# Performance work log

Measured on AMD Instinct MI355X. Metric: run time of the kernel, lower is better.

The kernel has to match this reference:

```python
import jax, jax.numpy as jnp
import numpy as np

B, K, N = 131072, 512, 1024  # batch, message bits, code bits


def setup_inputs() -> dict:
    key = jax.random.key(0)
    k1, k2 = jax.random.split(key)
    input_data = jax.random.randint(k1, (B, K), 0, 2).astype(jnp.float32)
    generator_matrix = jax.random.randint(k2, (N, K), 0, 2).astype(jnp.float32)
    return {"input_data": input_data, "generator_matrix": generator_matrix}


def reference(input_data, generator_matrix):
    # GF(2) encoding: (x @ G^T) mod 2
    # input_data: [B, K], generator_matrix: [N, K] -> out [B, N]
    prod = jnp.matmul(input_data, generator_matrix.T)
    return jnp.mod(prod, 2.0)
```

## Files before the change

### kernel.cpp

```cpp
#include <hip/hip_runtime.h>
#include <cstdint>


typedef float f32x4 __attribute__((ext_vector_type(4)));

__global__ void pack256_kernel(const float* __restrict__ in,
                               unsigned long long* __restrict__ out,
                               int nChunks) {
    const int chunk = blockIdx.x * (blockDim.x >> 6) + (threadIdx.x >> 6);
    const int lane = threadIdx.x & 63;
    if (chunk >= nChunks) return;
    const float4 v =
        reinterpret_cast<const float4*>(in + (size_t)chunk * 256)[lane];
    unsigned long long m0 = __ballot(v.x != 0.0f);
    unsigned long long m1 = __ballot(v.y != 0.0f);
    unsigned long long m2 = __ballot(v.z != 0.0f);
    unsigned long long m3 = __ballot(v.w != 0.0f);
    if (lane == 0) {
        unsigned long long* o = out + (size_t)chunk * 4;
        o[0] = m0; o[1] = m1; o[2] = m2; o[3] = m3;
    }
}

__global__ __launch_bounds__(256, 4) void gf2_fused_kernel(
    const float* __restrict__ x,
    const uint32_t* __restrict__ gp,
    float* __restrict__ out) {
    const int tid = threadIdx.x;
    const int lane = tid & 63;
    const long long b0 = (long long)blockIdx.x * 64;

    uint32_t g[4][16];
#pragma unroll
    for (int j = 0; j < 4; ++j) {
        const uint4* gr =
            reinterpret_cast<const uint4*>(gp + (size_t)(tid * 4 + j) * 16);
        uint4 a = gr[0], b = gr[1], c = gr[2], d = gr[3];
        g[j][0] = a.x;  g[j][1] = a.y;  g[j][2] = a.z;  g[j][3] = a.w;
        g[j][4] = b.x;  g[j][5] = b.y;  g[j][6] = b.z;  g[j][7] = b.w;
        g[j][8] = c.x;  g[j][9] = c.y;  g[j][10] = c.z; g[j][11] = c.w;
        g[j][12] = d.x; g[j][13] = d.y; g[j][14] = d.z; g[j][15] = d.w;
    }

    const float* xr = x + b0 * 512 + lane * 4;
    float4 p0 = *reinterpret_cast<const float4*>(xr);
    float4 p1 = *reinterpret_cast<const float4*>(xr + 256);

    for (int r = 0; r < 64; ++r) {
        const float4 c0 = p0, c1 = p1;
        if (r < 63) {
            xr += 512;
            p0 = *reinterpret_cast<const float4*>(xr);
            p1 = *reinterpret_cast<const float4*>(xr + 256);
        }
        unsigned long long m0 = __ballot(c0.x != 0.0f);
        unsigned long long m1 = __ballot(c0.y != 0.0f);
        unsigned long long m2 = __ballot(c0.z != 0.0f);
        unsigned long long m3 = __ballot(c0.w != 0.0f);
        unsigned long long m4 = __ballot(c1.x != 0.0f);
        unsigned long long m5 = __ballot(c1.y != 0.0f);
        unsigned long long m6 = __ballot(c1.z != 0.0f);
        unsigned long long m7 = __ballot(c1.w != 0.0f);
        const uint32_t xv[16] = {
            (uint32_t)m0, (uint32_t)(m0 >> 32),
            (uint32_t)m1, (uint32_t)(m1 >> 32),
            (uint32_t)m2, (uint32_t)(m2 >> 32),
            (uint32_t)m3, (uint32_t)(m3 >> 32),
            (uint32_t)m4, (uint32_t)(m4 >> 32),
            (uint32_t)m5, (uint32_t)(m5 >> 32),
            (uint32_t)m6, (uint32_t)(m6 >> 32),
            (uint32_t)m7, (uint32_t)(m7 >> 32)};

        uint32_t a0 = 0, a1 = 0, a2 = 0, a3 = 0;
#pragma unroll
        for (int i = 0; i < 16; ++i) {
            a0 ^= xv[i] & g[0][i];
            a1 ^= xv[i] & g[1][i];
            a2 ^= xv[i] & g[2][i];
            a3 ^= xv[i] & g[3][i];
        }
        f32x4 o;
        o.x = (float)(__popc(a0) & 1);
        o.y = (float)(__popc(a1) & 1);
        o.z = (float)(__popc(a2) & 1);
        o.w = (float)(__popc(a3) & 1);
        __builtin_nontemporal_store(
            o, reinterpret_cast<f32x4*>(out + (size_t)(b0 + r) * 1024) + tid);
    }
}

extern "C" void kernel_launch(void* const* d_in, const int* in_sizes, int n_in,
                              void* d_out, int out_size, void* d_ws, size_t ws_size,
                              hipStream_t stream) {
    const float* x = (const float*)d_in[0];
    const float* G = (const float*)d_in[1];
    float* out = (float*)d_out;

    const int B = 131072;
    unsigned long long* gp64 = (unsigned long long*)d_ws;

    pack256_kernel<<<512, 256, 0, stream>>>(G, gp64, 2048);
    gf2_fused_kernel<<<B / 64, 256, 0, stream>>>(
        x, (const uint32_t*)gp64, out);
}
```

Before: 187.4 us.

## Share bit-packed input rows across waves via LDS instead of redundant loads

Previously every wave in a block loaded and ballot-packed all 64 input rows, so each row was read from global memory four times. Now each wave packs a disjoint 16-row slice into shared memory, the block synchronizes, and all waves read the packed words from LDS for the XOR/AND loop. This cuts global and L2 read traffic for x by four, at the cost of a block barrier and losing overlap of loads with compute inside a wave.

```diff
diff --git a/kernel.cpp b/kernel.cpp
--- a/kernel.cpp
+++ b/kernel.cpp
@@ -26,8 +26,11 @@
     const float* __restrict__ x,
     const uint32_t* __restrict__ gp,
     float* __restrict__ out) {
+    __shared__ uint32_t xl[64 * 16];
+
     const int tid = threadIdx.x;
     const int lane = tid & 63;
+    const int wv = tid >> 6;
     const long long b0 = (long long)blockIdx.x * 64;
 
     uint32_t g[4][16];
@@ -42,35 +45,47 @@
         g[j][12] = d.x; g[j][13] = d.y; g[j][14] = d.z; g[j][15] = d.w;
     }
 
-    const float* xr = x + b0 * 512 + lane * 4;
-    float4 p0 = *reinterpret_cast<const float4*>(xr);
-    float4 p1 = *reinterpret_cast<const float4*>(xr + 256);
+    {
+        const float* xr = x + (b0 + wv * 16) * 512 + lane * 4;
+        float4 p0 = *reinterpret_cast<const float4*>(xr);
+        float4 p1 = *reinterpret_cast<const float4*>(xr + 256);
+        for (int r = 0; r < 16; ++r) {
+            const float4 c0 = p0, c1 = p1;
+            if (r < 15) {
+                xr += 512;
+                p0 = *reinterpret_cast<const float4*>(xr);
+                p1 = *reinterpret_cast<const float4*>(xr + 256);
+            }
+            unsigned long long m0 = __ballot(c0.x != 0.0f);
+            unsigned long long m1 = __ballot(c0.y != 0.0f);
+            unsigned long long m2 = __ballot(c0.z != 0.0f);
+            unsigned long long m3 = __ballot(c0.w != 0.0f);
+            unsigned long long m4 = __ballot(c1.x != 0.0f);
+            unsigned long long m5 = __ballot(c1.y != 0.0f);
+            unsigned long long m6 = __ballot(c1.z != 0.0f);
+            unsigned long long m7 = __ballot(c1.w != 0.0f);
+            if (lane == 0) {
+                uint4* dst = reinterpret_cast<uint4*>(&xl[(wv * 16 + r) * 16]);
+                dst[0] = make_uint4((uint32_t)m0, (uint32_t)(m0 >> 32),
+                                    (uint32_t)m1, (uint32_t)(m1 >> 32));
+                dst[1] = make_uint4((uint32_t)m2, (uint32_t)(m2 >> 32),
+                                    (uint32_t)m3, (uint32_t)(m3 >> 32));
+                dst[2] = make_uint4((uint32_t)m4, (uint32_t)(m4 >> 32),
+                                    (uint32_t)m5, (uint32_t)(m5 >> 32));
+                dst[3] = make_uint4((uint32_t)m6, (uint32_t)(m6 >> 32),
+                                    (uint32_t)m7, (uint32_t)(m7 >> 32));
+            }
+        }
+    }
+    __syncthreads();
 
     for (int r = 0; r < 64; ++r) {
-        const float4 c0 = p0, c1 = p1;
-        if (r < 63) {
-            xr += 512;
-            p0 = *reinterpret_cast<const float4*>(xr);
-            p1 = *reinterpret_cast<const float4*>(xr + 256);
-        }
-        unsigned long long m0 = __ballot(c0.x != 0.0f);
-        unsigned long long m1 = __ballot(c0.y != 0.0f);
-        unsigned long long m2 = __ballot(c0.z != 0.0f);
-        unsigned long long m3 = __ballot(c0.w != 0.0f);
-        unsigned long long m4 = __ballot(c1.x != 0.0f);
-        unsigned long long m5 = __ballot(c1.y != 0.0f);
-        unsigned long long m6 = __ballot(c1.z != 0.0f);
-        unsigned long long m7 = __ballot(c1.w != 0.0f);
-        const uint32_t xv[16] = {
-            (uint32_t)m0, (uint32_t)(m0 >> 32),
-            (uint32_t)m1, (uint32_t)(m1 >> 32),
-            (uint32_t)m2, (uint32_t)(m2 >> 32),
-            (uint32_t)m3, (uint32_t)(m3 >> 32),
-            (uint32_t)m4, (uint32_t)(m4 >> 32),
-            (uint32_t)m5, (uint32_t)(m5 >> 32),
-            (uint32_t)m6, (uint32_t)(m6 >> 32),
-            (uint32_t)m7, (uint32_t)(m7 >> 32)};
-
+        const uint4* xr4 = reinterpret_cast<const uint4*>(&xl[r * 16]);
+        uint4 q0 = xr4[0], q1 = xr4[1], q2 = xr4[2], q3 = xr4[3];
+        const uint32_t xv[16] = {q0.x, q0.y, q0.z, q0.w,
+                                 q1.x, q1.y, q1.z, q1.w,
+                                 q2.x, q2.y, q2.z, q2.w,
+                                 q3.x, q3.y, q3.z, q3.w};
         uint32_t a0 = 0, a1 = 0, a2 = 0, a3 = 0;
 #pragma unroll
         for (int i = 0; i < 16; ++i) {
```

After: 159.3 us. 1.18x faster.
